# Kernel optimization log

Measured on AMD Instinct MI355X. Metric: run time of the kernel, lower is better.

## Reference

```python
import jax, jax.numpy as jnp
import numpy as np

D_MODEL = 128
NUM_HEADS = 4
D_HEAD = 32
ATTN_COEFF = 0.5
BATCH = 2
SEQ = 4096


def setup_inputs() -> dict:
    key = jax.random.key(0)
    k1, k2, k3, k4, k5 = jax.random.split(key, 5)
    std = 1.0 / np.sqrt(D_MODEL)
    x = jax.random.normal(k1, (BATCH, SEQ, D_MODEL), dtype=jnp.float32)
    W_K = jax.random.normal(k2, (NUM_HEADS, D_HEAD, D_MODEL), dtype=jnp.float32) * std
    W_Q = jax.random.normal(k3, (NUM_HEADS, D_HEAD, D_MODEL), dtype=jnp.float32) * std
    W_V = jax.random.normal(k4, (NUM_HEADS, D_HEAD, D_MODEL), dtype=jnp.float32) * std
    W_O = jax.random.normal(k5, (D_MODEL, NUM_HEADS * D_HEAD), dtype=jnp.float32) * std
    return {"x": x, "W_K": W_K, "W_Q": W_Q, "W_V": W_V, "W_O": W_O}


def reference(x, W_K, W_Q, W_V, W_O):
    batch, seq, _ = x.shape
    # projections: [B, H, S, Dh]
    k = jnp.einsum('ihd,bpd->biph', W_K, x)
    q = jnp.einsum('ihd,bpd->biph', W_Q, x)
    v = jnp.einsum('ihd,bpd->biph', W_V, x)
    # scores: [B, H, Sq, Sk]
    scores = jnp.einsum('biph,biqh->biqp', k, q) / np.sqrt(D_HEAD).astype(np.float32)
    # NOTE: original code builds a causal mask but never applies it; faithful omission.
    attn = jax.nn.softmax(scores, axis=-1)
    # post-softmax affine blend with uniform offset
    attn = attn * ATTN_COEFF + (1.0 - ATTN_COEFF)
    z = jnp.einsum('biph,biqp->biqh', v, attn)          # [B, H, S, Dh]
    z_flat = jnp.transpose(z, (0, 2, 1, 3)).reshape(batch, seq, NUM_HEADS * D_HEAD)
    out = jnp.einsum('df,bpf->bpd', W_O, z_flat)        # [B, S, D]
    return out
```

## Files before the change

### kernel.cpp

```cpp
#include <hip/hip_runtime.h>

#define SQ 4096
#define NB 2
#define NH 4
#define DH 32
#define DM 128

typedef float f32x16 __attribute__((ext_vector_type(16)));
typedef float f32x4  __attribute__((ext_vector_type(4)));
typedef __bf16 bf16x8 __attribute__((ext_vector_type(8)));
typedef unsigned int uint4v __attribute__((ext_vector_type(4)));
typedef unsigned short u16;

union B8 { uint4v u; bf16x8 b; };

__device__ inline u16 f2bf(float x) {
  unsigned u = __builtin_bit_cast(unsigned, x);
  unsigned r = (u + 0x7FFF + ((u >> 16) & 1)) >> 16;
  return (u16)r;
}

__device__ inline float bf2f(u16 v) {
  return __builtin_bit_cast(float, (unsigned)v << 16);
}

__device__ inline unsigned cvt_pk_bf16(float a, float b) {
  unsigned r;
  asm("v_cvt_pk_bf16_f32 %0, %1, %2" : "=v"(r) : "v"(a), "v"(b));
  return r;
}

__device__ inline void swap32(unsigned &a, unsigned &b) {
  asm("v_permlane32_swap_b32 %0, %1" : "+v"(a), "+v"(b));
}

#if __has_builtin(__builtin_amdgcn_exp2f)
#define EX2 __builtin_amdgcn_exp2f
#else
#define EX2 exp2f
#endif

__device__ inline float xhalf_max(float x) {
  unsigned ua = __builtin_bit_cast(unsigned, x), ub = ua;
  asm("v_permlane32_swap_b32 %0, %1" : "+v"(ua), "+v"(ub));
  return fmaxf(__builtin_bit_cast(float, ua), __builtin_bit_cast(float, ub));
}

__device__ inline float xhalf_add(float x) {
  unsigned ua = __builtin_bit_cast(unsigned, x), ub = ua;
  asm("v_permlane32_swap_b32 %0, %1" : "+v"(ua), "+v"(ub));
  return __builtin_bit_cast(float, ua) + __builtin_bit_cast(float, ub);
}

__device__ inline float tmax16(const f32x16& v) {
  float a0 = fmaxf(v[0], v[1]), a1 = fmaxf(v[2], v[3]);
  float a2 = fmaxf(v[4], v[5]), a3 = fmaxf(v[6], v[7]);
  float a4 = fmaxf(v[8], v[9]), a5 = fmaxf(v[10], v[11]);
  float a6 = fmaxf(v[12], v[13]), a7 = fmaxf(v[14], v[15]);
  float b0 = fmaxf(a0, a1), b1 = fmaxf(a2, a3);
  float b2 = fmaxf(a4, a5), b3 = fmaxf(a6, a7);
  return fmaxf(fmaxf(b0, b1), fmaxf(b2, b3));
}

__global__ __launch_bounds__(256) void kprep(const float* __restrict__ x,
                                             const float* __restrict__ Wk,
                                             const float* __restrict__ Wq,
                                             const float* __restrict__ Wv,
                                             const float* __restrict__ Wo,
                                             u16* __restrict__ xb,
                                             u16* __restrict__ wb,
                                             float* __restrict__ woT,
                                             float* __restrict__ xsum) {
  const int bid = blockIdx.x, t = threadIdx.x;
  if (bid < 256) {
    const size_t base = (size_t)bid * 4096 + (size_t)t * 16;
    const f32x4* src = (const f32x4*)(x + base);
    uint4v* dst = (uint4v*)(xb + base);
    f32x4 v0 = src[0], v1 = src[1], v2 = src[2], v3 = src[3];
    uint4v o0, o1;
    o0[0] = cvt_pk_bf16(v0[0], v0[1]); o0[1] = cvt_pk_bf16(v0[2], v0[3]);
    o0[2] = cvt_pk_bf16(v1[0], v1[1]); o0[3] = cvt_pk_bf16(v1[2], v1[3]);
    o1[0] = cvt_pk_bf16(v2[0], v2[1]); o1[1] = cvt_pk_bf16(v2[2], v2[3]);
    o1[2] = cvt_pk_bf16(v3[0], v3[1]); o1[3] = cvt_pk_bf16(v3[2], v3[3]);
    dst[0] = o0; dst[1] = o1;
  } else if (bid < 384) {
    const int j = bid - 256;
    const int b = j >> 6, rblk = j & 63;
    const int d = t & 127, rh = t >> 7;
    const float* xp = x + ((size_t)b * SQ + rblk * 64) * DM + d;
    float a = 0.f;
    for (int r = rh; r < 64; r += 2) a += xp[(size_t)r * DM];
    __shared__ float red[2][DM];
    red[rh][d] = a;
    __syncthreads();
    if (t < DM) atomicAdd(&xsum[b * DM + t], red[0][t] + red[1][t]);
  } else {
    const int m = bid - 384;
    if (m < 3) {
      const float* W = (m == 0) ? Wk : (m == 1 ? Wq : Wv);
      const float s = (m == 1) ? (1.4426950408889634f / 5.656854249492380f) : 1.0f;
      for (int i = t; i < DM * DM; i += 256) wb[m * DM * DM + i] = f2bf(W[i] * s);
    } else {
      for (int i = t; i < DM * DM; i += 256) woT[(i & 127) * DM + (i >> 7)] = Wo[i];
    }
  }
}

__global__ __launch_bounds__(256) void kprojc(const u16* __restrict__ xb,
                                              const u16* __restrict__ wb,
                                              const float* __restrict__ Wv,
                                              const float* __restrict__ Wo,
                                              const float* __restrict__ xsum,
                                              u16* __restrict__ qb,
                                              u16* __restrict__ kb,
                                              u16* __restrict__ vt,
                                              float* __restrict__ cvec) {
  const int by = blockIdx.y;
  const int t = threadIdx.x;
  if (by == 12) {
    if (blockIdx.x >= NB) return;
    const int b = blockIdx.x;
    __shared__ float xs[DM], vs[DM];
    if (t < DM) xs[t] = xsum[b * DM + t];
    __syncthreads();
    const int c = t >> 1, half = t & 1;
    float a = 0.f;
    const float* wr = Wv + c * DM + half * 64;
    const float* xh = xs + half * 64;
    for (int i = 0; i < 64; ++i) a += wr[i] * xh[i];
    a += __shfl_xor(a, 1, 64);
    if (half == 0) vs[c] = a;
    __syncthreads();
    float a2 = 0.f;
    const float* wr2 = Wo + c * DM + half * 64;
    const float* vh = vs + half * 64;
    for (int i = 0; i < 64; ++i) a2 += wr2[i] * vh[i];
    a2 += __shfl_xor(a2, 1, 64);
    if (half == 0) cvec[b * DM + c] = 0.5f * a2;
    return;
  }
  const int lane = t & 63, wid = t >> 6;
  const int l31 = lane & 31, hi = lane >> 5;
  const int mat = by >> 2, h = by & 3;
  const int p0 = (blockIdx.x * 4 + wid) * 32;
  const u16* xrow = xb + (size_t)(p0 + l31) * DM + 8 * hi;
  const u16* wrow = wb + mat * DM * DM + (h * 32 + l31) * DM + 8 * hi;
  f32x16 acc;
#pragma unroll
  for (int r = 0; r < 16; ++r) acc[r] = 0.f;
#pragma unroll
  for (int ks = 0; ks < 8; ++ks) {
    B8 a, w;
    a.u = *(const uint4v*)(xrow + ks * 16);
    w.u = *(const uint4v*)(wrow + ks * 16);
    acc = __builtin_amdgcn_mfma_f32_32x32x16_bf16(a.b, w.b, acc, 0, 0, 0);
  }
  const int b = p0 >> 12, pl = p0 & (SQ - 1);
  const size_t bh = (size_t)b * NH + h;
  if (mat < 2) {
    u16* dst = (mat ? qb : kb) + (bh * SQ + pl) * DH + l31;
#pragma unroll
    for (int r = 0; r < 16; ++r) {
      int row = (r & 3) + 8 * (r >> 2) + 4 * hi;
      dst[(size_t)row * DH] = f2bf(acc[r]);
    }
  } else {
    u16* dst = vt + ((bh * (SQ / 32) + (pl >> 5)) * DH + l31) * 32;
#pragma unroll
    for (int r = 0; r < 16; ++r) {
      int row = (r & 3) + 8 * (r >> 2) + 4 * hi;
      dst[row] = f2bf(acc[r]);
    }
  }
}

#define SOFTMAX_PV(SC, M, S, ACC, V0, V1) {                                    \
  float p_[16];                                                                \
  _Pragma("unroll") for (int r = 0; r < 16; ++r) p_[r] = EX2(SC[r] - M);       \
  float ls = ((p_[0]+p_[1])+(p_[2]+p_[3]))+((p_[4]+p_[5])+(p_[6]+p_[7]));      \
  ls += ((p_[8]+p_[9])+(p_[10]+p_[11]))+((p_[12]+p_[13])+(p_[14]+p_[15]));     \
  S += xhalf_add(ls);                                                          \
  unsigned w0 = cvt_pk_bf16(p_[0], p_[1]),  w1 = cvt_pk_bf16(p_[2], p_[3]);    \
  unsigned w2 = cvt_pk_bf16(p_[4], p_[5]),  w3 = cvt_pk_bf16(p_[6], p_[7]);    \
  unsigned w4 = cvt_pk_bf16(p_[8], p_[9]),  w5 = cvt_pk_bf16(p_[10], p_[11]);  \
  unsigned w6 = cvt_pk_bf16(p_[12], p_[13]), w7 = cvt_pk_bf16(p_[14], p_[15]); \
  swap32(w0, w2); swap32(w1, w3); swap32(w4, w6); swap32(w5, w7);              \
  B8 bp0_, bp1_;                                                               \
  bp0_.u[0] = w0; bp0_.u[1] = w1; bp0_.u[2] = w2; bp0_.u[3] = w3;              \
  bp1_.u[0] = w4; bp1_.u[1] = w5; bp1_.u[2] = w6; bp1_.u[3] = w7;              \
  ACC = __builtin_amdgcn_mfma_f32_32x32x16_bf16(V0.b, bp0_.b, ACC, 0, 0, 0);   \
  ACC = __builtin_amdgcn_mfma_f32_32x32x16_bf16(V1.b, bp1_.b, ACC, 0, 0, 0);   \
}

#define TILE(K0, K1, V0, V1, NOFF) {                                             \
  f32x16 sc0 = __builtin_amdgcn_mfma_f32_32x32x16_bf16(K0.b, qf00.b, zacc, 0,0,0); \
  sc0 = __builtin_amdgcn_mfma_f32_32x32x16_bf16(K1.b, qf01.b, sc0, 0, 0, 0);     \
  f32x16 sc1 = __builtin_amdgcn_mfma_f32_32x32x16_bf16(K0.b, qf10.b, zacc, 0,0,0); \
  sc1 = __builtin_amdgcn_mfma_f32_32x32x16_bf16(K1.b, qf11.b, sc1, 0, 0, 0);     \
  K0.u = *(const uint4v*)(kT + (NOFF));                                          \
  K1.u = *(const uint4v*)(kT + (NOFF) + 16);                                     \
  float pm0 = xhalf_max(tmax16(sc0));                                            \
  float pm1 = xhalf_max(tmax16(sc1));                                            \
  if (__any((pm0 > m0 + 8.f) | (pm1 > m1 + 8.f))) {                              \
    float n0 = fmaxf(m0, pm0), n1 = fmaxf(m1, pm1);                              \
    float r0 = EX2(m0 - n0), r1 = EX2(m1 - n1);                                  \
    s0 *= r0; s1 *= r1;                                                          \
    _Pragma("unroll") for (int r = 0; r < 16; ++r) { acc0[r] *= r0; acc1[r] *= r1; } \
    m0 = n0; m1 = n1;                                                            \
  }                                                                              \
  SOFTMAX_PV(sc0, m0, s0, acc0, V0, V1)                                          \
  SOFTMAX_PV(sc1, m1, s1, acc1, V0, V1)                                          \
  V0.u = *(const uint4v*)(vT + (NOFF));                                          \
  V1.u = *(const uint4v*)(vT + (NOFF) + 16);                                     \
}

__global__ __launch_bounds__(256) void kattn(const u16* __restrict__ qb,
                                             const u16* __restrict__ kb,
                                             const u16* __restrict__ vt,
                                             u16* __restrict__ yT) {
  __shared__ float sm_[3][2][64], ss_[3][2][64], sa_[3][2][16][64];
  const int t = threadIdx.x, lane = t & 63, wid = t >> 6;
  const int l31 = lane & 31, hi = lane >> 5;
  const int bh = blockIdx.y;
  const int qbase = blockIdx.x * 64;

  const u16* qrow0 = qb + ((size_t)bh * SQ + qbase + l31) * DH + 8 * hi;
  const u16* qrow1 = qrow0 + 32 * DH;
  B8 qf00, qf01, qf10, qf11;
  qf00.u = *(const uint4v*)(qrow0);
  qf01.u = *(const uint4v*)(qrow0 + 16);
  qf10.u = *(const uint4v*)(qrow1);
  qf11.u = *(const uint4v*)(qrow1 + 16);

  const int kh = wid;
  const u16* kT = kb + ((size_t)bh * SQ + kh * 1024) * DH + l31 * 32 + 8 * hi;
  const u16* vT = vt + ((size_t)bh * (SQ / 32) + kh * 32) * (DH * 32) + l31 * 32 + 8 * hi;

  f32x16 zacc, acc0, acc1;
#pragma unroll
  for (int r = 0; r < 16; ++r) { zacc[r] = 0.f; acc0[r] = 0.f; acc1[r] = 0.f; }
  float m0 = -1e30f, m1 = -1e30f, s0 = 0.f, s1 = 0.f;

  B8 ka0, ka1, va0, va1, kb0, kb1, vb0, vb1;
  ka0.u = *(const uint4v*)(kT);        ka1.u = *(const uint4v*)(kT + 16);
  va0.u = *(const uint4v*)(vT);        va1.u = *(const uint4v*)(vT + 16);
  kb0.u = *(const uint4v*)(kT + 1024); kb1.u = *(const uint4v*)(kT + 1024 + 16);
  vb0.u = *(const uint4v*)(vT + 1024); vb1.u = *(const uint4v*)(vT + 1024 + 16);

  for (int ti = 0; ti < 32; ti += 2) {
    const int off = ti << 10;
    TILE(ka0, ka1, va0, va1, off + 2048)
    TILE(kb0, kb1, vb0, vb1, off + 3072)
  }

  if (wid) {
    const int w = wid - 1;
    sm_[w][0][lane] = m0; sm_[w][1][lane] = m1;
    ss_[w][0][lane] = s0; ss_[w][1][lane] = s1;
#pragma unroll
    for (int r = 0; r < 16; ++r) { sa_[w][0][r][lane] = acc0[r]; sa_[w][1][r][lane] = acc1[r]; }
  }
  __syncthreads();
  if (wid == 0) {
#pragma unroll
    for (int g = 0; g < 2; ++g) {
      float m = g ? m1 : m0, s = g ? s1 : s0;
      float mm = m;
#pragma unroll
      for (int w = 0; w < 3; ++w) mm = fmaxf(mm, sm_[w][g][lane]);
      float e = EX2(m - mm);
      float den = s * e;
      float ew[3];
#pragma unroll
      for (int w = 0; w < 3; ++w) {
        ew[w] = EX2(sm_[w][g][lane] - mm);
        den += ss_[w][g][lane] * ew[w];
      }
      float inv = 0.5f / den;
      u16* yp = yT + (size_t)bh * 32 * SQ + qbase + g * 32 + l31;
#pragma unroll
      for (int r = 0; r < 16; ++r) {
        float o = (g ? acc1[r] : acc0[r]) * e;
#pragma unroll
        for (int w = 0; w < 3; ++w) o += sa_[w][g][r][lane] * ew[w];
        int row = (r & 3) + 8 * (r >> 2) + 4 * hi;
        yp[(size_t)row * SQ] = f2bf(o * inv);
      }
    }
  }
}

__global__ __launch_bounds__(256) void kout(const u16* __restrict__ yT,
                                            const float* __restrict__ woT,
                                            const float* __restrict__ cvec,
                                            float* __restrict__ out) {
  __shared__ float yS[DM][16];
  const int t = threadIdx.x;
  const int b = blockIdx.y;
  const int P0 = blockIdx.x * 16;
  for (int idx = t; idx < DM * 16; idx += 256) {
    int f = idx >> 4, p = idx & 15;
    yS[f][p] = bf2f(yT[((size_t)b * DM + f) * SQ + P0 + p]);
  }
  __syncthreads();
  const int d4 = (t & 31) * 4;
  const int pg = (t >> 5) * 2;
  f32x4 a0 = {0.f, 0.f, 0.f, 0.f}, a1 = {0.f, 0.f, 0.f, 0.f};
  for (int f = 0; f < DM; ++f) {
    f32x4 wv = *(const f32x4*)&woT[f * DM + d4];
    float y0 = yS[f][pg], y1 = yS[f][pg + 1];
    a0 += wv * y0;
    a1 += wv * y1;
  }
  f32x4 cv = *(const f32x4*)&cvec[b * DM + d4];
  a0 += cv; a1 += cv;
  *(f32x4*)&out[((size_t)b * SQ + P0 + pg) * DM + d4] = a0;
  *(f32x4*)&out[((size_t)b * SQ + P0 + pg + 1) * DM + d4] = a1;
}

extern "C" void kernel_launch(void* const* d_in, const int* in_sizes, int n_in,
                              void* d_out, int out_size, void* d_ws, size_t ws_size,
                              hipStream_t stream) {
  const float* x  = (const float*)d_in[0];
  const float* Wk = (const float*)d_in[1];
  const float* Wq = (const float*)d_in[2];
  const float* Wv = (const float*)d_in[3];
  const float* Wo = (const float*)d_in[4];
  float* out = (float*)d_out;
  char* ws = (char*)d_ws;
  float* woT  = (float*)(ws);
  float* xsum = (float*)(ws + (64 << 10));
  float* cvec = (float*)(ws + (68 << 10));
  u16* wb = (u16*)(ws + (80 << 10));
  u16* qb = (u16*)(ws + (256 << 10));
  u16* kb = (u16*)(ws + (256 << 10) + ((size_t)2 << 20));
  u16* vt = (u16*)(ws + (256 << 10) + ((size_t)4 << 20));
  u16* yT = (u16*)(ws + (256 << 10) + ((size_t)6 << 20));
  u16* xb = yT;

  hipMemsetAsync(xsum, 0, NB * DM * sizeof(float), stream);
  kprep<<<dim3(388), dim3(256), 0, stream>>>(x, Wk, Wq, Wv, Wo, xb, wb, woT, xsum);
  kprojc<<<dim3(64, 13), dim3(256), 0, stream>>>(xb, wb, Wv, Wo, xsum, qb, kb, vt, cvec);
  kattn<<<dim3(64, 8), dim3(256), 0, stream>>>(qb, kb, vt, yT);
  kout<<<dim3(256, 2), dim3(256), 0, stream>>>(yT, woT, cvec, out);
}
```

Measured before the change: 141.7 us.

## Halve attention query tile per block and move output projection onto bf16 MFMA

The attention kernel now processes 32 queries per block instead of 64, doubling the grid to 1024 blocks with a launch-bounds occupancy hint, and writes its output row-major [B,S,128] rather than transposed. The output projection becomes an MFMA bf16 GEMM that reads W_O converted to bf16 in the prep kernel, replacing the fp32 scalar FMA loop and the W_O transpose. tmax16 also gets a different reduction tree. More blocks per CU is meant to give more parallelism and latency hiding, at the cost of re-reading K/V twice as often and adding bf16 rounding of W_O.

```diff
diff --git a/kernel.cpp b/kernel.cpp
--- a/kernel.cpp
+++ b/kernel.cpp
@@ -20,10 +20,6 @@
   return (u16)r;
 }
 
-__device__ inline float bf2f(u16 v) {
-  return __builtin_bit_cast(float, (unsigned)v << 16);
-}
-
 __device__ inline unsigned cvt_pk_bf16(float a, float b) {
   unsigned r;
   asm("v_cvt_pk_bf16_f32 %0, %1, %2" : "=v"(r) : "v"(a), "v"(b));
@@ -53,13 +49,14 @@
 }
 
 __device__ inline float tmax16(const f32x16& v) {
-  float a0 = fmaxf(v[0], v[1]), a1 = fmaxf(v[2], v[3]);
-  float a2 = fmaxf(v[4], v[5]), a3 = fmaxf(v[6], v[7]);
-  float a4 = fmaxf(v[8], v[9]), a5 = fmaxf(v[10], v[11]);
-  float a6 = fmaxf(v[12], v[13]), a7 = fmaxf(v[14], v[15]);
-  float b0 = fmaxf(a0, a1), b1 = fmaxf(a2, a3);
-  float b2 = fmaxf(a4, a5), b3 = fmaxf(a6, a7);
-  return fmaxf(fmaxf(b0, b1), fmaxf(b2, b3));
+  float a0 = fmaxf(fmaxf(v[0], v[1]), v[2]);
+  float a1 = fmaxf(fmaxf(v[3], v[4]), v[5]);
+  float a2 = fmaxf(fmaxf(v[6], v[7]), v[8]);
+  float a3 = fmaxf(fmaxf(v[9], v[10]), v[11]);
+  float a4 = fmaxf(fmaxf(v[12], v[13]), v[14]);
+  float b0 = fmaxf(fmaxf(a0, a1), a2);
+  float b1 = fmaxf(fmaxf(a3, a4), v[15]);
+  return fmaxf(b0, b1);
 }
 
 __global__ __launch_bounds__(256) void kprep(const float* __restrict__ x,
@@ -69,7 +66,6 @@
                                              const float* __restrict__ Wo,
                                              u16* __restrict__ xb,
                                              u16* __restrict__ wb,
-                                             float* __restrict__ woT,
                                              float* __restrict__ xsum) {
   const int bid = blockIdx.x, t = threadIdx.x;
   if (bid < 256) {
@@ -101,7 +97,7 @@
       const float s = (m == 1) ? (1.4426950408889634f / 5.656854249492380f) : 1.0f;
       for (int i = t; i < DM * DM; i += 256) wb[m * DM * DM + i] = f2bf(W[i] * s);
     } else {
-      for (int i = t; i < DM * DM; i += 256) woT[(i & 127) * DM + (i >> 7)] = Wo[i];
+      for (int i = t; i < DM * DM; i += 256) wb[3 * DM * DM + i] = f2bf(Wo[i]);
     }
   }
 }
@@ -174,72 +170,61 @@
   }
 }
 
-#define SOFTMAX_PV(SC, M, S, ACC, V0, V1) {                                    \
-  float p_[16];                                                                \
-  _Pragma("unroll") for (int r = 0; r < 16; ++r) p_[r] = EX2(SC[r] - M);       \
-  float ls = ((p_[0]+p_[1])+(p_[2]+p_[3]))+((p_[4]+p_[5])+(p_[6]+p_[7]));      \
-  ls += ((p_[8]+p_[9])+(p_[10]+p_[11]))+((p_[12]+p_[13])+(p_[14]+p_[15]));     \
-  S += xhalf_add(ls);                                                          \
-  unsigned w0 = cvt_pk_bf16(p_[0], p_[1]),  w1 = cvt_pk_bf16(p_[2], p_[3]);    \
-  unsigned w2 = cvt_pk_bf16(p_[4], p_[5]),  w3 = cvt_pk_bf16(p_[6], p_[7]);    \
-  unsigned w4 = cvt_pk_bf16(p_[8], p_[9]),  w5 = cvt_pk_bf16(p_[10], p_[11]);  \
-  unsigned w6 = cvt_pk_bf16(p_[12], p_[13]), w7 = cvt_pk_bf16(p_[14], p_[15]); \
-  swap32(w0, w2); swap32(w1, w3); swap32(w4, w6); swap32(w5, w7);              \
-  B8 bp0_, bp1_;                                                               \
-  bp0_.u[0] = w0; bp0_.u[1] = w1; bp0_.u[2] = w2; bp0_.u[3] = w3;              \
-  bp1_.u[0] = w4; bp1_.u[1] = w5; bp1_.u[2] = w6; bp1_.u[3] = w7;              \
-  ACC = __builtin_amdgcn_mfma_f32_32x32x16_bf16(V0.b, bp0_.b, ACC, 0, 0, 0);   \
-  ACC = __builtin_amdgcn_mfma_f32_32x32x16_bf16(V1.b, bp1_.b, ACC, 0, 0, 0);   \
-}
-
-#define TILE(K0, K1, V0, V1, NOFF) {                                             \
-  f32x16 sc0 = __builtin_amdgcn_mfma_f32_32x32x16_bf16(K0.b, qf00.b, zacc, 0,0,0); \
-  sc0 = __builtin_amdgcn_mfma_f32_32x32x16_bf16(K1.b, qf01.b, sc0, 0, 0, 0);     \
-  f32x16 sc1 = __builtin_amdgcn_mfma_f32_32x32x16_bf16(K0.b, qf10.b, zacc, 0,0,0); \
-  sc1 = __builtin_amdgcn_mfma_f32_32x32x16_bf16(K1.b, qf11.b, sc1, 0, 0, 0);     \
-  K0.u = *(const uint4v*)(kT + (NOFF));                                          \
-  K1.u = *(const uint4v*)(kT + (NOFF) + 16);                                     \
-  float pm0 = xhalf_max(tmax16(sc0));                                            \
-  float pm1 = xhalf_max(tmax16(sc1));                                            \
-  if (__any((pm0 > m0 + 8.f) | (pm1 > m1 + 8.f))) {                              \
-    float n0 = fmaxf(m0, pm0), n1 = fmaxf(m1, pm1);                              \
-    float r0 = EX2(m0 - n0), r1 = EX2(m1 - n1);                                  \
-    s0 *= r0; s1 *= r1;                                                          \
-    _Pragma("unroll") for (int r = 0; r < 16; ++r) { acc0[r] *= r0; acc1[r] *= r1; } \
-    m0 = n0; m1 = n1;                                                            \
-  }                                                                              \
-  SOFTMAX_PV(sc0, m0, s0, acc0, V0, V1)                                          \
-  SOFTMAX_PV(sc1, m1, s1, acc1, V0, V1)                                          \
-  V0.u = *(const uint4v*)(vT + (NOFF));                                          \
-  V1.u = *(const uint4v*)(vT + (NOFF) + 16);                                     \
-}
-
-__global__ __launch_bounds__(256) void kattn(const u16* __restrict__ qb,
-                                             const u16* __restrict__ kb,
-                                             const u16* __restrict__ vt,
-                                             u16* __restrict__ yT) {
-  __shared__ float sm_[3][2][64], ss_[3][2][64], sa_[3][2][16][64];
+#define TILE(K0, K1, V0, V1, NOFF) {                                               \
+  f32x16 sc = __builtin_amdgcn_mfma_f32_32x32x16_bf16(K0.b, qf0.b, zacc, 0, 0, 0); \
+  sc = __builtin_amdgcn_mfma_f32_32x32x16_bf16(K1.b, qf1.b, sc, 0, 0, 0);          \
+  K0.u = *(const uint4v*)(kT + (NOFF));                                            \
+  K1.u = *(const uint4v*)(kT + (NOFF) + 16);                                       \
+  float pm = xhalf_max(tmax16(sc));                                                \
+  if (__any(pm > m + 8.f)) {                                                       \
+    float n = fmaxf(m, pm);                                                        \
+    float rs = EX2(m - n);                                                         \
+    s *= rs;                                                                       \
+    _Pragma("unroll") for (int r = 0; r < 16; ++r) acc[r] *= rs;                   \
+    m = n;                                                                         \
+  }                                                                                \
+  float p_[16];                                                                    \
+  _Pragma("unroll") for (int r = 0; r < 16; ++r) p_[r] = EX2(sc[r] - m);           \
+  float ls = ((p_[0]+p_[1])+(p_[2]+p_[3]))+((p_[4]+p_[5])+(p_[6]+p_[7]));          \
+  ls += ((p_[8]+p_[9])+(p_[10]+p_[11]))+((p_[12]+p_[13])+(p_[14]+p_[15]));         \
+  s += xhalf_add(ls);                                                              \
+  unsigned w0 = cvt_pk_bf16(p_[0], p_[1]),  w1 = cvt_pk_bf16(p_[2], p_[3]);        \
+  unsigned w2 = cvt_pk_bf16(p_[4], p_[5]),  w3 = cvt_pk_bf16(p_[6], p_[7]);        \
+  unsigned w4 = cvt_pk_bf16(p_[8], p_[9]),  w5 = cvt_pk_bf16(p_[10], p_[11]);      \
+  unsigned w6 = cvt_pk_bf16(p_[12], p_[13]), w7 = cvt_pk_bf16(p_[14], p_[15]);     \
+  swap32(w0, w2); swap32(w1, w3); swap32(w4, w6); swap32(w5, w7);                  \
+  B8 bp0_, bp1_;                                                                   \
+  bp0_.u[0] = w0; bp0_.u[1] = w1; bp0_.u[2] = w2; bp0_.u[3] = w3;                  \
+  bp1_.u[0] = w4; bp1_.u[1] = w5; bp1_.u[2] = w6; bp1_.u[3] = w7;                  \
+  acc = __builtin_amdgcn_mfma_f32_32x32x16_bf16(V0.b, bp0_.b, acc, 0, 0, 0);       \
+  acc = __builtin_amdgcn_mfma_f32_32x32x16_bf16(V1.b, bp1_.b, acc, 0, 0, 0);       \
+  V0.u = *(const uint4v*)(vT + (NOFF));                                            \
+  V1.u = *(const uint4v*)(vT + (NOFF) + 16);                                       \
+}
+
+__global__ __launch_bounds__(256, 4) void kattn(const u16* __restrict__ qb,
+                                                const u16* __restrict__ kb,
+                                                const u16* __restrict__ vt,
+                                                u16* __restrict__ yb) {
+  __shared__ float sm_[3][64], ss_[3][64], sa_[3][16][64];
   const int t = threadIdx.x, lane = t & 63, wid = t >> 6;
   const int l31 = lane & 31, hi = lane >> 5;
   const int bh = blockIdx.y;
-  const int qbase = blockIdx.x * 64;
-
-  const u16* qrow0 = qb + ((size_t)bh * SQ + qbase + l31) * DH + 8 * hi;
-  const u16* qrow1 = qrow0 + 32 * DH;
-  B8 qf00, qf01, qf10, qf11;
-  qf00.u = *(const uint4v*)(qrow0);
-  qf01.u = *(const uint4v*)(qrow0 + 16);
-  qf10.u = *(const uint4v*)(qrow1);
-  qf11.u = *(const uint4v*)(qrow1 + 16);
+  const int qbase = blockIdx.x * 32;
+
+  const u16* qrow = qb + ((size_t)bh * SQ + qbase + l31) * DH + 8 * hi;
+  B8 qf0, qf1;
+  qf0.u = *(const uint4v*)(qrow);
+  qf1.u = *(const uint4v*)(qrow + 16);
 
   const int kh = wid;
   const u16* kT = kb + ((size_t)bh * SQ + kh * 1024) * DH + l31 * 32 + 8 * hi;
   const u16* vT = vt + ((size_t)bh * (SQ / 32) + kh * 32) * (DH * 32) + l31 * 32 + 8 * hi;
 
-  f32x16 zacc, acc0, acc1;
-#pragma unroll
-  for (int r = 0; r < 16; ++r) { zacc[r] = 0.f; acc0[r] = 0.f; acc1[r] = 0.f; }
-  float m0 = -1e30f, m1 = -1e30f, s0 = 0.f, s1 = 0.f;
+  f32x16 zacc, acc;
+#pragma unroll
+  for (int r = 0; r < 16; ++r) { zacc[r] = 0.f; acc[r] = 0.f; }
+  float m = -1e30f, s = 0.f;
 
   B8 ka0, ka1, va0, va1, kb0, kb1, vb0, vb1;
   ka0.u = *(const uint4v*)(kT);        ka1.u = *(const uint4v*)(kT + 16);
@@ -255,67 +240,67 @@
 
   if (wid) {
     const int w = wid - 1;
-    sm_[w][0][lane] = m0; sm_[w][1][lane] = m1;
-    ss_[w][0][lane] = s0; ss_[w][1][lane] = s1;
-#pragma unroll
-    for (int r = 0; r < 16; ++r) { sa_[w][0][r][lane] = acc0[r]; sa_[w][1][r][lane] = acc1[r]; }
+    sm_[w][lane] = m;
+    ss_[w][lane] = s;
+#pragma unroll
+    for (int r = 0; r < 16; ++r) sa_[w][r][lane] = acc[r];
   }
   __syncthreads();
   if (wid == 0) {
-#pragma unroll
-    for (int g = 0; g < 2; ++g) {
-      float m = g ? m1 : m0, s = g ? s1 : s0;
-      float mm = m;
-#pragma unroll
-      for (int w = 0; w < 3; ++w) mm = fmaxf(mm, sm_[w][g][lane]);
-      float e = EX2(m - mm);
-      float den = s * e;
-      float ew[3];
-#pragma unroll
-      for (int w = 0; w < 3; ++w) {
-        ew[w] = EX2(sm_[w][g][lane] - mm);
-        den += ss_[w][g][lane] * ew[w];
-      }
-      float inv = 0.5f / den;
-      u16* yp = yT + (size_t)bh * 32 * SQ + qbase + g * 32 + l31;
-#pragma unroll
-      for (int r = 0; r < 16; ++r) {
-        float o = (g ? acc1[r] : acc0[r]) * e;
-#pragma unroll
-        for (int w = 0; w < 3; ++w) o += sa_[w][g][r][lane] * ew[w];
-        int row = (r & 3) + 8 * (r >> 2) + 4 * hi;
-        yp[(size_t)row * SQ] = f2bf(o * inv);
-      }
-    }
-  }
-}
-
-__global__ __launch_bounds__(256) void kout(const u16* __restrict__ yT,
-                                            const float* __restrict__ woT,
+    float mm = m;
+#pragma unroll
+    for (int w = 0; w < 3; ++w) mm = fmaxf(mm, sm_[w][lane]);
+    float e = EX2(m - mm);
+    float den = s * e;
+    float ew[3];
+#pragma unroll
+    for (int w = 0; w < 3; ++w) {
+      ew[w] = EX2(sm_[w][lane] - mm);
+      den += ss_[w][lane] * ew[w];
+    }
+    float inv = 0.5f / den;
+    const int b = bh >> 2, h = bh & 3;
+    u16* yp = yb + ((size_t)(b * SQ) + qbase + l31) * DM + h * 32;
+#pragma unroll
+    for (int r = 0; r < 16; ++r) {
+      float o = acc[r] * e;
+#pragma unroll
+      for (int w = 0; w < 3; ++w) o += sa_[w][r][lane] * ew[w];
+      int row = (r & 3) + 8 * (r >> 2) + 4 * hi;
+      yp[row] = f2bf(o * inv);
+    }
+  }
+}
+
+__global__ __launch_bounds__(256) void kout(const u16* __restrict__ yb,
+                                            const u16* __restrict__ wob,
                                             const float* __restrict__ cvec,
                                             float* __restrict__ out) {
-  __shared__ float yS[DM][16];
-  const int t = threadIdx.x;
-  const int b = blockIdx.y;
-  const int P0 = blockIdx.x * 16;
-  for (int idx = t; idx < DM * 16; idx += 256) {
-    int f = idx >> 4, p = idx & 15;
-    yS[f][p] = bf2f(yT[((size_t)b * DM + f) * SQ + P0 + p]);
-  }
-  __syncthreads();
-  const int d4 = (t & 31) * 4;
-  const int pg = (t >> 5) * 2;
-  f32x4 a0 = {0.f, 0.f, 0.f, 0.f}, a1 = {0.f, 0.f, 0.f, 0.f};
-  for (int f = 0; f < DM; ++f) {
-    f32x4 wv = *(const f32x4*)&woT[f * DM + d4];
-    float y0 = yS[f][pg], y1 = yS[f][pg + 1];
-    a0 += wv * y0;
-    a1 += wv * y1;
-  }
-  f32x4 cv = *(const f32x4*)&cvec[b * DM + d4];
-  a0 += cv; a1 += cv;
-  *(f32x4*)&out[((size_t)b * SQ + P0 + pg) * DM + d4] = a0;
-  *(f32x4*)&out[((size_t)b * SQ + P0 + pg + 1) * DM + d4] = a1;
+  const int t = threadIdx.x, lane = t & 63, wid = t >> 6;
+  const int l31 = lane & 31, hi = lane >> 5;
+  const int blk = blockIdx.x;
+  const int b = blk >> 7;
+  const int p0 = (blk & 127) * 32;
+  const int d0 = wid * 32;
+  const u16* yrow = yb + ((size_t)(b * SQ) + p0 + l31) * DM + 8 * hi;
+  const u16* wrow = wob + (size_t)(d0 + l31) * DM + 8 * hi;
+  f32x16 acc;
+#pragma unroll
+  for (int r = 0; r < 16; ++r) acc[r] = 0.f;
+#pragma unroll
+  for (int ks = 0; ks < 8; ++ks) {
+    B8 a, w;
+    a.u = *(const uint4v*)(yrow + ks * 16);
+    w.u = *(const uint4v*)(wrow + ks * 16);
+    acc = __builtin_amdgcn_mfma_f32_32x32x16_bf16(a.b, w.b, acc, 0, 0, 0);
+  }
+  float cv = cvec[b * DM + d0 + l31];
+  float* op = out + ((size_t)(b * SQ) + p0) * DM + d0 + l31;
+#pragma unroll
+  for (int r = 0; r < 16; ++r) {
+    int row = (r & 3) + 8 * (r >> 2) + 4 * hi;
+    op[(size_t)row * DM] = acc[r] + cv;
+  }
 }
 
 extern "C" void kernel_launch(void* const* d_in, const int* in_sizes, int n_in,
@@ -328,19 +313,18 @@
   const float* Wo = (const float*)d_in[4];
   float* out = (float*)d_out;
   char* ws = (char*)d_ws;
-  float* woT  = (float*)(ws);
-  float* xsum = (float*)(ws + (64 << 10));
-  float* cvec = (float*)(ws + (68 << 10));
-  u16* wb = (u16*)(ws + (80 << 10));
+  float* xsum = (float*)(ws);
+  float* cvec = (float*)(ws + (4 << 10));
+  u16* wb = (u16*)(ws + (64 << 10));
   u16* qb = (u16*)(ws + (256 << 10));
   u16* kb = (u16*)(ws + (256 << 10) + ((size_t)2 << 20));
   u16* vt = (u16*)(ws + (256 << 10) + ((size_t)4 << 20));
-  u16* yT = (u16*)(ws + (256 << 10) + ((size_t)6 << 20));
-  u16* xb = yT;
+  u16* yb = (u16*)(ws + (256 << 10) + ((size_t)6 << 20));
+  u16* xb = yb;
 
   hipMemsetAsync(xsum, 0, NB * DM * sizeof(float), stream);
-  kprep<<<dim3(388), dim3(256), 0, stream>>>(x, Wk, Wq, Wv, Wo, xb, wb, woT, xsum);
+  kprep<<<dim3(388), dim3(256), 0, stream>>>(x, Wk, Wq, Wv, Wo, xb, wb, xsum);
   kprojc<<<dim3(64, 13), dim3(256), 0, stream>>>(xb, wb, Wv, Wo, xsum, qb, kb, vt, cvec);
-  kattn<<<dim3(64, 8), dim3(256), 0, stream>>>(qb, kb, vt, yT);
-  kout<<<dim3(256, 2), dim3(256), 0, stream>>>(yT, woT, cvec, out);
-}
+  kattn<<<dim3(128, 8), dim3(256), 0, stream>>>(qb, kb, vt, yb);
+  kout<<<dim3(256), dim3(256), 0, stream>>>(yb, wb + 3 * DM * DM, cvec, out);
+}
```

Result: faster. 124.3 us (-12.3%).
